# Kernel optimization log

Hardware: AMD Instinct MI355X
Metric: run time of the kernel (lower is better)

Reference implementation:

```python
import jax, jax.numpy as jnp
import numpy as np

N_BINS = 32
EPS = 6.4 / 256.0
LO = -3.2 - EPS / 2.0
HI = 3.2 - EPS / 2.0
BIN_W = (HI - LO) / N_BINS


def _rgb_uv_hist_one(img):
    # img: [3, H, W] -> [3, 32, 32] sqrt-normalized RGB-uv histogram
    C, H, W = img.shape
    # cv2 INTER_NEAREST downsample: src index = floor(dst * scale)
    ry = jnp.floor(jnp.arange(N_BINS) * (H / N_BINS)).astype(jnp.int32)
    rx = jnp.floor(jnp.arange(N_BINS) * (W / N_BINS)).astype(jnp.int32)
    small = img[:, ry][:, :, rx]                 # [3, 32, 32]
    px = small.reshape(3, -1)                    # [3, 1024]
    valid = jnp.all(px > 0, axis=0)              # pixels with all channels > 0
    Iy = jnp.sqrt(jnp.sum(px * px, axis=0))      # per-pixel L2 norm (weights)
    w = jnp.where(valid, Iy, 0.0)
    px_safe = jnp.where(px > 0, px, 1.0)         # guard log for masked pixels
    logs = jnp.log(px_safe)                      # [3, 1024]
    hists = []
    for i in range(3):
        r = [j for j in range(3) if j != i]
        Iu = logs[i] - logs[r[1]]
        Iv = logs[i] - logs[r[0]]
        inb = valid & (Iu >= LO) & (Iu <= HI) & (Iv >= LO) & (Iv <= HI)
        iu = jnp.clip(jnp.floor((Iu - LO) / BIN_W).astype(jnp.int32), 0, N_BINS - 1)
        iv = jnp.clip(jnp.floor((Iv - LO) / BIN_W).astype(jnp.int32), 0, N_BINS - 1)
        flat = iu * N_BINS + iv                  # histogram2d: rows=Iu, cols=Iv
        h = jnp.zeros(N_BINS * N_BINS, dtype=px.dtype).at[flat].add(jnp.where(inb, w, 0.0))
        h = h / jnp.sum(h)
        hists.append(jnp.sqrt(h).reshape(N_BINS, N_BINS))
    return jnp.stack(hists)                      # [3, 32, 32]


def setup_inputs() -> dict:
    key = jax.random.key(0)
    ks = jax.random.split(key, 7)
    B, H, W = 32, 512, 512
    inp_img = jax.random.uniform(ks[0], (B, 3, H, W), dtype=jnp.float32)
    s = 0.02
    return {
        "inp_img": inp_img,
        "W1": jax.random.normal(ks[1], (1024, 3072), jnp.float32) * s,
        "b1": jax.random.normal(ks[2], (1024,), jnp.float32) * s,
        "W2": jax.random.normal(ks[3], (512, 1024), jnp.float32) * s,
        "b2": jax.random.normal(ks[4], (512,), jnp.float32) * s,
        "W3": jax.random.normal(ks[5], (256, 512), jnp.float32) * s,
        "b3": jax.random.normal(ks[6], (256,), jnp.float32) * s,
    }


def reference(inp_img, W1, b1, W2, b2, W3, b3):
    B = inp_img.shape[0]
    hist = jax.vmap(_rgb_uv_hist_one)(inp_img).reshape(B, -1)  # [B, 3072]
    hist = jax.lax.stop_gradient(hist)  # original code detaches the histogram
    x = jax.nn.relu(hist @ W1.T + b1)
    x = jax.nn.relu(x @ W2.T + b2)
    x = jax.nn.relu(x @ W3.T + b3)      # [B, 256]
    return x[..., None, None]            # [B, 256, 1, 1]
```

## Files before the change

### kernel.cpp

```cpp
#include <hip/hip_runtime.h>
#include <math.h>

#define IMG_H 512
#define IMG_W 512
#define HWSZ (IMG_H * IMG_W)
#define BATCH 32

__device__ __forceinline__ size_t xidx(int k, int b) {
    return (size_t)(k >> 1) * 64 + b * 2 + (k & 1);
}

__global__ __launch_bounds__(256) void hist_part_k(const float* __restrict__ img,
                                                   float* __restrict__ hp,
                                                   const float* __restrict__ b1,
                                                   const float* __restrict__ b2,
                                                   const float* __restrict__ b3,
                                                   float* __restrict__ y1,
                                                   float* __restrict__ y2,
                                                   float* __restrict__ y3)
{
    if (blockIdx.x >= 128) {
        const int t = (blockIdx.x - 128) * 256 + threadIdx.x;
        if (t < 32768) {
            const int o = ((t >> 6) << 1) | (t & 1);
            y1[t] = b1[o];
        } else if (t < 49152) {
            const int u = t - 32768;
            const int o = ((u >> 6) << 1) | (u & 1);
            y2[u] = b2[o];
        } else {
            const int u = t - 49152;
            const int o = ((u >> 6) << 1) | (u & 1);
            y3[u] = b3[o];
        }
        return;
    }

    const int img_i = blockIdx.x >> 2;
    const int blk   = blockIdx.x & 3;
    const int tid   = threadIdx.x;

    __shared__ float hh[3072];
    for (int i = tid; i < 3072; i += 256) hh[i] = 0.f;
    __syncthreads();

    const int p  = blk * 256 + tid;
    const int py = p >> 5;
    const int px = p & 31;
    const size_t base = (size_t)img_i * 3 * HWSZ + (size_t)(py * 16) * IMG_W + (size_t)(px * 16);

    const float r  = img[base];
    const float g  = img[base + HWSZ];
    const float bl = img[base + 2 * HWSZ];

    const bool valid = (r > 0.f) && (g > 0.f) && (bl > 0.f);

    const float LOc = (float)(-3.2 - (6.4 / 256.0) * 0.5);
    const float HIc = (float)( 3.2 - (6.4 / 256.0) * 0.5);
    const float BWc = (float)(((3.2 - (6.4 / 256.0) * 0.5) - (-3.2 - (6.4 / 256.0) * 0.5)) / 32.0);

    if (valid) {
        const float w  = sqrtf(r * r + g * g + bl * bl);
        const float lr = logf(r);
        const float lg = logf(g);
        const float lb = logf(bl);

        float us[3] = { lr - lb, lg - lb, lb - lg };
        float vs[3] = { lr - lg, lg - lr, lb - lr };

        #pragma unroll
        for (int i = 0; i < 3; ++i) {
            const float U = us[i];
            const float V = vs[i];
            if (U >= LOc && U <= HIc && V >= LOc && V <= HIc) {
                int iu = (int)floorf((U - LOc) / BWc); iu = iu < 31 ? iu : 31;
                int iv = (int)floorf((V - LOc) / BWc); iv = iv < 31 ? iv : 31;
                atomicAdd(&hh[i * 1024 + iu * 32 + iv], w);
            }
        }
    }
    __syncthreads();

    float* outp = hp + (size_t)blockIdx.x * 3072;
    for (int i = tid; i < 3072; i += 256) outp[i] = hh[i];
}

__global__ __launch_bounds__(1024) void hist_norm_k(const float* __restrict__ hp,
                                                    float* __restrict__ histT)
{
    const int img_i = blockIdx.x;
    const int tid   = threadIdx.x;
    const int wid   = tid >> 6;
    const int lane  = tid & 63;

    __shared__ float red[17];
    const float* base = hp + (size_t)img_i * 4 * 3072;

    #pragma unroll
    for (int c = 0; c < 3; ++c) {
        const int idx = c * 1024 + tid;
        float v = base[idx] + base[3072 + idx] + base[2 * 3072 + idx] + base[3 * 3072 + idx];

        float t = v;
        #pragma unroll
        for (int off = 32; off; off >>= 1) t += __shfl_down(t, off);
        if (lane == 0) red[wid] = t;
        __syncthreads();
        if (tid == 0) {
            float s = 0.f;
            #pragma unroll
            for (int j = 0; j < 16; ++j) s += red[j];
            red[16] = s;
        }
        __syncthreads();
        const float s = red[16];
        histT[xidx(c * 1024 + tid, img_i)] = sqrtf(v / s);
        __syncthreads();
    }
}

template <int K, int N, int S, bool RELU>
__global__ __launch_bounds__(256) void gemm_atomic_k(const float* __restrict__ xT,
                                                     const float* __restrict__ W,
                                                     float* __restrict__ y)
{
    constexpr int C  = K / S;
    constexpr int NG = N / 8;

    const int wave = (blockIdx.x * 256 + threadIdx.x) >> 6;
    const int lane = threadIdx.x & 63;
    const int b    = lane & 31;
    const int o0   = __builtin_amdgcn_readfirstlane((wave % NG) * 8);
    const int k0   = __builtin_amdgcn_readfirstlane((wave / NG) * C);

    const float* Wr[8];
    #pragma unroll
    for (int j = 0; j < 8; ++j) Wr[j] = W + (size_t)(o0 + j) * K + k0;

    const float2* xp = reinterpret_cast<const float2*>(xT + (size_t)k0 * BATCH) + b;

    float acc[8] = {0.f, 0.f, 0.f, 0.f, 0.f, 0.f, 0.f, 0.f};

    #pragma unroll 4
    for (int kk2 = 0; kk2 < C / 2; ++kk2) {
        float2 v = xp[kk2 * BATCH];
        if (RELU) { v.x = fmaxf(v.x, 0.f); v.y = fmaxf(v.y, 0.f); }
        #pragma unroll
        for (int j = 0; j < 8; ++j) {
            acc[j] = fmaf(v.x, Wr[j][2 * kk2],     acc[j]);
            acc[j] = fmaf(v.y, Wr[j][2 * kk2 + 1], acc[j]);
        }
    }

    if (lane < 32) {
        #pragma unroll
        for (int j = 0; j < 8; ++j)
            atomicAdd(&y[xidx(o0 + j, b)], acc[j]);
    }
}

__global__ __launch_bounds__(256) void finish_k(const float* __restrict__ y3,
                                                float* __restrict__ out)
{
    const int t = blockIdx.x * 256 + threadIdx.x;
    const int b = t >> 8;
    const int o = t & 255;
    out[t] = fmaxf(y3[xidx(o, b)], 0.f);
}

extern "C" void kernel_launch(void* const* d_in, const int* in_sizes, int n_in,
                              void* d_out, int out_size, void* d_ws, size_t ws_size,
                              hipStream_t stream)
{
    const float* img = (const float*)d_in[0];
    const float* W1  = (const float*)d_in[1];
    const float* b1  = (const float*)d_in[2];
    const float* W2  = (const float*)d_in[3];
    const float* b2  = (const float*)d_in[4];
    const float* W3  = (const float*)d_in[5];
    const float* b3  = (const float*)d_in[6];
    float* out = (float*)d_out;

    float* ws = (float*)d_ws;
    float* hp    = ws;
    float* histT = hp    + 128 * 3072;
    float* y1    = histT + 3072 * BATCH;
    float* y2    = y1    + 1024 * BATCH;
    float* y3    = y2    +  512 * BATCH;

    hist_part_k<<<128 + 224, 256, 0, stream>>>(img, hp, b1, b2, b3, y1, y2, y3);
    hist_norm_k<<<BATCH, 1024, 0, stream>>>(hp, histT);

    gemm_atomic_k<3072, 1024, 16, false><<<512, 256, 0, stream>>>(histT, W1, y1);
    gemm_atomic_k<1024,  512, 16, true ><<<256, 256, 0, stream>>>(y1, W2, y2);
    gemm_atomic_k< 512,  256, 16, true ><<<128, 256, 0, stream>>>(y2, W3, y3);

    finish_k<<<32, 256, 0, stream>>>(y3, out);
}
```

Measured before the change: 188.6 us.

## Fuse histogram normalization into one kernel and fold last layer with output

```diff
diff --git a/kernel.cpp b/kernel.cpp
--- a/kernel.cpp
+++ b/kernel.cpp
@@ -10,44 +10,40 @@
     return (size_t)(k >> 1) * 64 + b * 2 + (k & 1);
 }
 
-__global__ __launch_bounds__(256) void hist_part_k(const float* __restrict__ img,
-                                                   float* __restrict__ hp,
-                                                   const float* __restrict__ b1,
-                                                   const float* __restrict__ b2,
-                                                   const float* __restrict__ b3,
-                                                   float* __restrict__ y1,
-                                                   float* __restrict__ y2,
-                                                   float* __restrict__ y3)
-{
-    if (blockIdx.x >= 128) {
-        const int t = (blockIdx.x - 128) * 256 + threadIdx.x;
-        if (t < 32768) {
+__global__ __launch_bounds__(1024) void hist_bias_k(const float* __restrict__ img,
+                                                    float* __restrict__ histT,
+                                                    const float* __restrict__ b1,
+                                                    const float* __restrict__ b2,
+                                                    float* __restrict__ y1,
+                                                    float* __restrict__ y2)
+{
+    if (blockIdx.x >= 32) {
+        const int t = (blockIdx.x - 32) * 1024 + threadIdx.x;
+        {
             const int o = ((t >> 6) << 1) | (t & 1);
             y1[t] = b1[o];
-        } else if (t < 49152) {
-            const int u = t - 32768;
-            const int o = ((u >> 6) << 1) | (u & 1);
-            y2[u] = b2[o];
-        } else {
-            const int u = t - 49152;
-            const int o = ((u >> 6) << 1) | (u & 1);
-            y3[u] = b3[o];
+        }
+        if (t < 16384) {
+            const int o = ((t >> 6) << 1) | (t & 1);
+            y2[t] = b2[o];
         }
         return;
     }
 
-    const int img_i = blockIdx.x >> 2;
-    const int blk   = blockIdx.x & 3;
-    const int tid   = threadIdx.x;
-
-    __shared__ float hh[3072];
-    for (int i = tid; i < 3072; i += 256) hh[i] = 0.f;
+    const int b   = blockIdx.x;
+    const int tid = threadIdx.x;
+
+    __shared__ float hh[3][1024];
+    __shared__ float red[17];
+
+    hh[0][tid] = 0.f;
+    hh[1][tid] = 0.f;
+    hh[2][tid] = 0.f;
     __syncthreads();
 
-    const int p  = blk * 256 + tid;
-    const int py = p >> 5;
-    const int px = p & 31;
-    const size_t base = (size_t)img_i * 3 * HWSZ + (size_t)(py * 16) * IMG_W + (size_t)(px * 16);
+    const int py  = tid >> 5;
+    const int pxi = tid & 31;
+    const size_t base = (size_t)b * 3 * HWSZ + (size_t)(py * 16) * IMG_W + (size_t)(pxi * 16);
 
     const float r  = img[base];
     const float g  = img[base + HWSZ];
@@ -75,46 +71,29 @@
             if (U >= LOc && U <= HIc && V >= LOc && V <= HIc) {
                 int iu = (int)floorf((U - LOc) / BWc); iu = iu < 31 ? iu : 31;
                 int iv = (int)floorf((V - LOc) / BWc); iv = iv < 31 ? iv : 31;
-                atomicAdd(&hh[i * 1024 + iu * 32 + iv], w);
+                atomicAdd(&hh[i][iu * 32 + iv], w);
             }
         }
     }
     __syncthreads();
 
-    float* outp = hp + (size_t)blockIdx.x * 3072;
-    for (int i = tid; i < 3072; i += 256) outp[i] = hh[i];
-}
-
-__global__ __launch_bounds__(1024) void hist_norm_k(const float* __restrict__ hp,
-                                                    float* __restrict__ histT)
-{
-    const int img_i = blockIdx.x;
-    const int tid   = threadIdx.x;
-    const int wid   = tid >> 6;
-    const int lane  = tid & 63;
-
-    __shared__ float red[17];
-    const float* base = hp + (size_t)img_i * 4 * 3072;
-
     #pragma unroll
-    for (int c = 0; c < 3; ++c) {
-        const int idx = c * 1024 + tid;
-        float v = base[idx] + base[3072 + idx] + base[2 * 3072 + idx] + base[3 * 3072 + idx];
-
+    for (int i = 0; i < 3; ++i) {
+        float v = hh[i][tid];
         float t = v;
         #pragma unroll
         for (int off = 32; off; off >>= 1) t += __shfl_down(t, off);
-        if (lane == 0) red[wid] = t;
+        if ((tid & 63) == 0) red[tid >> 6] = t;
         __syncthreads();
         if (tid == 0) {
             float s = 0.f;
             #pragma unroll
             for (int j = 0; j < 16; ++j) s += red[j];
-            red[16] = s;
+            red[16] = 1.0f / s;
         }
         __syncthreads();
-        const float s = red[16];
-        histT[xidx(c * 1024 + tid, img_i)] = sqrtf(v / s);
+        const float inv = red[16];
+        histT[xidx(i * 1024 + tid, b)] = sqrtf(v * inv);
         __syncthreads();
     }
 }
@@ -159,13 +138,51 @@
     }
 }
 
-__global__ __launch_bounds__(256) void finish_k(const float* __restrict__ y3,
-                                                float* __restrict__ out)
-{
-    const int t = blockIdx.x * 256 + threadIdx.x;
-    const int b = t >> 8;
-    const int o = t & 255;
-    out[t] = fmaxf(y3[xidx(o, b)], 0.f);
+template <int K, int N>
+__global__ __launch_bounds__(256) void linear_out_k(const float* __restrict__ xT,
+                                                    const float* __restrict__ W,
+                                                    const float* __restrict__ bias,
+                                                    float* __restrict__ out)
+{
+    constexpr int C = K / 4;
+    const int og   = blockIdx.x;
+    const int w    = threadIdx.x >> 6;
+    const int lane = threadIdx.x & 63;
+    const int b    = lane & 31;
+    const int o0   = og * 8;
+    const int k0   = __builtin_amdgcn_readfirstlane(w * C);
+
+    const float* Wr[8];
+    #pragma unroll
+    for (int j = 0; j < 8; ++j) Wr[j] = W + (size_t)(o0 + j) * K + k0;
+
+    const float2* xp = reinterpret_cast<const float2*>(xT + (size_t)k0 * BATCH) + b;
+
+    float acc[8] = {0.f, 0.f, 0.f, 0.f, 0.f, 0.f, 0.f, 0.f};
+
+    #pragma unroll 4
+    for (int kk2 = 0; kk2 < C / 2; ++kk2) {
+        float2 v = xp[kk2 * BATCH];
+        v.x = fmaxf(v.x, 0.f); v.y = fmaxf(v.y, 0.f);
+        #pragma unroll
+        for (int j = 0; j < 8; ++j) {
+            acc[j] = fmaf(v.x, Wr[j][2 * kk2],     acc[j]);
+            acc[j] = fmaf(v.y, Wr[j][2 * kk2 + 1], acc[j]);
+        }
+    }
+
+    __shared__ float part[4][8][32];
+    if (lane < 32) {
+        #pragma unroll
+        for (int j = 0; j < 8; ++j) part[w][j][b] = acc[j];
+    }
+    __syncthreads();
+
+    const int j  = threadIdx.x >> 5;
+    const int b2 = threadIdx.x & 31;
+    float s = part[0][j][b2] + part[1][j][b2] + part[2][j][b2] + part[3][j][b2]
+            + bias[o0 + j];
+    out[b2 * N + o0 + j] = fmaxf(s, 0.f);
 }
 
 extern "C" void kernel_launch(void* const* d_in, const int* in_sizes, int n_in,
@@ -182,18 +199,13 @@
     float* out = (float*)d_out;
 
     float* ws = (float*)d_ws;
-    float* hp    = ws;
-    float* histT = hp    + 128 * 3072;
+    float* histT = ws;
     float* y1    = histT + 3072 * BATCH;
     float* y2    = y1    + 1024 * BATCH;
-    float* y3    = y2    +  512 * BATCH;
-
-    hist_part_k<<<128 + 224, 256, 0, stream>>>(img, hp, b1, b2, b3, y1, y2, y3);
-    hist_norm_k<<<BATCH, 1024, 0, stream>>>(hp, histT);
+
+    hist_bias_k<<<64, 1024, 0, stream>>>(img, histT, b1, b2, y1, y2);
 
     gemm_atomic_k<3072, 1024, 16, false><<<512, 256, 0, stream>>>(histT, W1, y1);
     gemm_atomic_k<1024,  512, 16, true ><<<256, 256, 0, stream>>>(y1, W2, y2);
-    gemm_atomic_k< 512,  256, 16, true ><<<128, 256, 0, stream>>>(y2, W3, y3);
-
-    finish_k<<<32, 256, 0, stream>>>(y3, out);
-}
+    linear_out_k<512, 256><<<32, 256, 0, stream>>>(y2, W3, b3, out);
+}
```

Measured after the change: 194.7 us. +3.2%, slower.
